# Optimization experiments

Hardware: AMD Instinct MI355X
Metric: run time of the kernel (lower is better)

## Reference

```python
import jax, jax.numpy as jnp
import numpy as np

N = 65536        # total nodes
E = 2097152      # total edges (avg degree 32)
B = 1024         # graphs / proteins
FXD = 78         # atom feature dim
DIM = 32         # GIN hidden dim
EMB = 128        # protein embedding dim
OUTD = 128       # output_dim
VOCAB = 26       # CHARPROTLEN + 1
PLEN = 1000      # protein sequence length (conv in_channels)
KS = 8           # conv kernel size
CLEN = EMB - KS + 1  # 121
NF = 32          # n_filters


def setup_inputs() -> dict:
    key = jax.random.key(0)
    ks = jax.random.split(key, 30)
    g = lambda k, s: (jax.random.normal(k, s, dtype=jnp.float32) * 0.05)
    inp = {
        "x": jax.random.normal(ks[0], (N, FXD), dtype=jnp.float32),
        "edge_index": jax.random.randint(ks[1], (2, E), 0, N, dtype=jnp.int32),
        "batch": jnp.sort(jax.random.randint(ks[2], (N,), 0, B, dtype=jnp.int32)),
        "target": jax.random.randint(ks[3], (B, PLEN), 0, VOCAB, dtype=jnp.int32),
        # GIN layer 1 MLP
        "w1a": g(ks[4], (FXD, DIM)), "b1a": jnp.zeros((DIM,), jnp.float32),
        "w1b": g(ks[5], (DIM, DIM)), "b1b": jnp.zeros((DIM,), jnp.float32),
        # GIN layers 2-5 MLPs (stacked)
        "wa": g(ks[6], (4, DIM, DIM)), "ba": jnp.zeros((4, DIM), jnp.float32),
        "wb": g(ks[7], (4, DIM, DIM)), "bb": jnp.zeros((4, DIM), jnp.float32),
        # BatchNorm affine params for bn1..bn5
        "gamma": jnp.ones((5, DIM), jnp.float32),
        "beta": jnp.zeros((5, DIM), jnp.float32),
        # drug head
        "w_fcxd": g(ks[8], (DIM, OUTD)), "b_fcxd": jnp.zeros((OUTD,), jnp.float32),
        # protein branch
        "emb": g(ks[9], (VOCAB, EMB)),
        "conv_w": g(ks[10], (NF, PLEN, KS)),  # OIH layout
        "conv_b": jnp.zeros((NF,), jnp.float32),
        "w_fcxt": g(ks[11], (NF * CLEN, OUTD)), "b_fcxt": jnp.zeros((OUTD,), jnp.float32),
        # joint head
        "w_fc1": g(ks[12], (256, 1024)), "b_fc1": jnp.zeros((1024,), jnp.float32),
        "w_fc2": g(ks[13], (1024, 256)), "b_fc2": jnp.zeros((256,), jnp.float32),
        "w_out": g(ks[14], (256, 1)), "b_out": jnp.zeros((1,), jnp.float32),
    }
    return inp


def reference(x, edge_index, batch, target,
              w1a, b1a, w1b, b1b, wa, ba, wb, bb, gamma, beta,
              w_fcxd, b_fcxd, emb, conv_w, conv_b, w_fcxt, b_fcxt,
              w_fc1, b_fc1, w_fc2, b_fc2, w_out, b_out):
    n_nodes = x.shape[0]
    n_graphs = target.shape[0]
    src, dst = edge_index[0], edge_index[1]

    def gin_bn(h, wi, bi, wo, bo, g, bt):
        # GINConv (eps=0): nn((1+eps)*x + sum_{j->i} x_j), then ReLU, then BatchNorm1d (batch stats)
        agg = jax.ops.segment_sum(h[src], dst, num_segments=n_nodes) + h
        h = jnp.maximum(agg @ wi + bi, 0.0) @ wo + bo
        h = jnp.maximum(h, 0.0)
        m = h.mean(axis=0)
        v = h.var(axis=0)  # biased, matches torch BN normalization
        return g * (h - m) * jax.lax.rsqrt(v + 1e-5) + bt

    h = gin_bn(x, w1a, b1a, w1b, b1b, gamma[0], beta[0])
    for i in range(4):
        h = gin_bn(h, wa[i], ba[i], wb[i], bb[i], gamma[i + 1], beta[i + 1])

    # global add pool over graphs
    hg = jax.ops.segment_sum(h, batch, num_segments=n_graphs)  # [B, 32]
    xd = jnp.maximum(hg @ w_fcxd + b_fcxd, 0.0)  # [B, 128] (dropout inactive in eval)

    # protein branch: embed then Conv1d over the embedding axis (in_channels = seq positions)
    e = emb[target]  # [B, 1000, 128]
    c = jax.lax.conv_general_dilated(e, conv_w, window_strides=(1,), padding="VALID",
                                     dimension_numbers=("NCH", "OIH", "NCH"))
    c = c + conv_b[None, :, None]  # [B, 32, 121]
    xt = c.reshape(n_graphs, NF * CLEN) @ w_fcxt + b_fcxt  # [B, 128], no activation in original

    xc = jnp.concatenate([xd, xt], axis=1)  # [B, 256]
    xc = jnp.maximum(xc @ w_fc1 + b_fc1, 0.0)
    xc = jnp.maximum(xc @ w_fc2 + b_fc2, 0.0)
    return xc @ w_out + b_out  # [B, 1]
```

## Files before the change

### kernel.cpp

```cpp
#include <hip/hip_runtime.h>
#include <hip/hip_fp16.h>

#define N_NODES 65536
#define N_EDGES 2097152
#define NB      1024
#define FXD     78
#define DIM     32
#define EMBD    128
#define OUTD    128
#define VOCAB   26
#define PLEN    1000
#define KS      8
#define CLEN    121
#define NF      32
#define FCX     (NF*CLEN)
#define NBKT    256
#define EPB     8192
#define NSLICE  256
#define EROW2   156
#define ECHUNK  13


__global__ __launch_bounds__(256) void k_bhist(
    const int* __restrict__ ei, int* __restrict__ bktCnt)
{
    __shared__ int h[NBKT];
    int tid = threadIdx.x;
    h[tid] = 0;
    __syncthreads();
    int base = blockIdx.x*1024;
    #pragma unroll
    for (int q=0; q<4; ++q) {
        int d = ei[N_EDGES + base + q*256 + tid];
        atomicAdd(&h[d>>8], 1);
    }
    __syncthreads();
    atomicAdd(&bktCnt[tid], h[tid]);
}

__global__ __launch_bounds__(256) void k_bscan(
    const int* __restrict__ bktCnt, int* __restrict__ bktBase, int* __restrict__ bktCur)
{
    __shared__ int s[NBKT];
    int t = threadIdx.x;
    int v = bktCnt[t];
    s[t] = v;
    __syncthreads();
    for (int off=1; off<256; off<<=1) {
        int tv = (t >= off) ? s[t-off] : 0;
        __syncthreads();
        s[t] += tv;
        __syncthreads();
    }
    int ex = s[t] - v;
    bktBase[t] = ex;
    bktCur[t] = ex;
    if (t == 255) bktBase[256] = s[255];
}

__global__ __launch_bounds__(256) void k_bucketA(
    const int* __restrict__ ei, int* __restrict__ bktCur, unsigned int* __restrict__ pairs)
{
    __shared__ unsigned int raw[EPB];
    __shared__ unsigned int srt[EPB];
    __shared__ unsigned char bOf[EPB];
    __shared__ int hist[NBKT], sc[NBKT], lcur[NBKT], gbase[NBKT];
    int tid = threadIdx.x;
    hist[tid] = 0;
    __syncthreads();
    int eb = blockIdx.x * EPB;
    for (int i=tid; i<EPB; i+=256) {
        int s = ei[eb+i];
        int d = ei[N_EDGES+eb+i];
        raw[i] = ((unsigned int)d<<16) | (unsigned int)s;
        atomicAdd(&hist[d>>8], 1);
    }
    __syncthreads();
    int v = hist[tid];
    sc[tid] = v;
    __syncthreads();
    for (int off=1; off<256; off<<=1) {
        int tv = (tid >= off) ? sc[tid-off] : 0;
        __syncthreads();
        sc[tid] += tv;
        __syncthreads();
    }
    int ex = sc[tid] - v;
    sc[tid] = ex;
    lcur[tid] = ex;
    gbase[tid] = atomicAdd(&bktCur[tid], v);
    __syncthreads();
    for (int i=tid; i<EPB; i+=256) {
        unsigned int p = raw[i];
        int k = p >> 24;
        int pos = atomicAdd(&lcur[k], 1);
        srt[pos] = p;
        bOf[pos] = (unsigned char)k;
    }
    __syncthreads();
    for (int i=tid; i<EPB; i+=256) {
        int k = bOf[i];
        pairs[gbase[k] + (i - sc[k])] = srt[i];
    }
}

__global__ __launch_bounds__(256) void k_fillB(
    const int* __restrict__ bktBase, const unsigned int* __restrict__ pairs,
    int* __restrict__ rowptr, int* __restrict__ csr)
{
    __shared__ int hist[256], sc[256], cur[256];
    int b = blockIdx.x, tid = threadIdx.x;
    int node0 = b*256;
    hist[tid] = 0;
    __syncthreads();
    int s = bktBase[b], e = bktBase[b+1];
    for (int i = s + tid; i < e; i += 256)
        atomicAdd(&hist[(pairs[i] >> 16) & 255], 1);
    __syncthreads();
    int v = hist[tid];
    sc[tid] = v;
    __syncthreads();
    for (int off=1; off<256; off<<=1) {
        int tv = (tid >= off) ? sc[tid-off] : 0;
        __syncthreads();
        sc[tid] += tv;
        __syncthreads();
    }
    int base = s + sc[tid] - v;
    rowptr[node0 + tid] = base;
    cur[tid] = base;
    if (b == NBKT-1 && tid == 255) rowptr[N_NODES] = N_EDGES;
    __syncthreads();
    for (int i = s + tid; i < e; i += 256) {
        unsigned int p = pairs[i];
        int pos = atomicAdd(&cur[(p >> 16) & 255], 1);
        csr[pos] = (int)(p & 0xFFFFu);
    }
}


__global__ __launch_bounds__(256) void k_l1_transform(
    const float* __restrict__ x, const float* __restrict__ w,
    __half* __restrict__ t)
{
    __shared__ float wS[FXD*DIM];
    for (int i = threadIdx.x; i < FXD*DIM; i += 256) wS[i] = w[i];
    __syncthreads();
    int node = blockIdx.x*256 + threadIdx.x;
    float acc[DIM];
    #pragma unroll
    for (int d=0; d<DIM; ++d) acc[d] = 0.f;
    const float* xr = x + (long)node*FXD;
    for (int j=0; j<FXD; ++j) {
        float xv = xr[j];
        #pragma unroll
        for (int d=0; d<DIM; ++d) acc[d] += xv * wS[j*DIM+d];
    }
    union { __half2 h2[16]; uint4 u4[4]; } pk;
    #pragma unroll
    for (int q=0; q<16; ++q) pk.h2[q] = __floats2half2_rn(acc[2*q], acc[2*q+1]);
    uint4* dst4 = (uint4*)(t + (long)node*DIM);
    #pragma unroll
    for (int q=0; q<4; ++q) dst4[q] = pk.u4[q];
}

__global__ __launch_bounds__(256) void k_transform(
    const float* __restrict__ z, const float* __restrict__ ss,
    const float* __restrict__ w, __half* __restrict__ t)
{
    __shared__ float wS[DIM*DIM];
    __shared__ float sS[2*DIM];
    for (int i = threadIdx.x; i < DIM*DIM; i += 256) wS[i] = w[i];
    if (threadIdx.x < 2*DIM) sS[threadIdx.x] = ss[threadIdx.x];
    __syncthreads();
    int node = blockIdx.x*256 + threadIdx.x;
    float h[DIM];
    const float4* z4 = (const float4*)(z + (long)node*DIM);
    #pragma unroll
    for (int q=0; q<DIM/4; ++q) {
        float4 v = z4[q];
        h[q*4+0]=v.x; h[q*4+1]=v.y; h[q*4+2]=v.z; h[q*4+3]=v.w;
    }
    #pragma unroll
    for (int d=0; d<DIM; ++d) h[d] = h[d]*sS[d] + sS[DIM+d];
    float acc[DIM];
    #pragma unroll
    for (int d=0; d<DIM; ++d) acc[d] = 0.f;
    #pragma unroll
    for (int j=0; j<DIM; ++j) {
        float hv = h[j];
        #pragma unroll
        for (int d=0; d<DIM; ++d) acc[d] += hv * wS[j*DIM+d];
    }
    union { __half2 h2[16]; uint4 u4[4]; } pk;
    #pragma unroll
    for (int q=0; q<16; ++q) pk.h2[q] = __floats2half2_rn(acc[2*q], acc[2*q+1]);
    uint4* dst4 = (uint4*)(t + (long)node*DIM);
    #pragma unroll
    for (int q=0; q<4; ++q) dst4[q] = pk.u4[q];
}

__global__ __launch_bounds__(256) void k_gather_mlp(
    const int* __restrict__ rowptr, const int* __restrict__ csr,
    const __half* __restrict__ t,
    const float* __restrict__ bi, const float* __restrict__ wo, const float* __restrict__ bo,
    float* __restrict__ z, float* __restrict__ part)
{
    __shared__ float wS[DIM*DIM];
    __shared__ float bS[2*DIM];
    __shared__ float stS[2*DIM];
    int tid = threadIdx.x;
    for (int i=tid; i<DIM*DIM; i+=256) wS[i]=wo[i];
    if (tid<DIM) bS[tid]=bi[tid];
    else if (tid<2*DIM) bS[tid]=bo[tid-DIM];
    if (tid<2*DIM) stS[tid]=0.f;
    __syncthreads();
    int g = tid >> 3;
    int l = tid & 7;
    int node = blockIdx.x*32 + g;
    const uint2* t4 = (const uint2*)t;
    uint2 sv = t4[(long)node*8 + l];
    float2 p0 = __half22float2(*(const __half2*)&sv.x);
    float2 p1 = __half22float2(*(const __half2*)&sv.y);
    float a0=p0.x, a1=p0.y, a2=p1.x, a3=p1.y;
    float c0=0.f, c1=0.f, c2=0.f, c3=0.f;
    int s0 = rowptr[node], s1 = rowptr[node+1];
    int e = s0;
    for (; e+8 <= s1; e+=8) {
        int myIdx = csr[e + l];
        #pragma unroll
        for (int k=0; k<8; ++k) {
            int idx = __shfl(myIdx, k, 8);
            uint2 v = t4[(long)idx*8 + l];
            float2 q0 = __half22float2(*(const __half2*)&v.x);
            float2 q1 = __half22float2(*(const __half2*)&v.y);
            if (k & 1) { c0+=q0.x; c1+=q0.y; c2+=q1.x; c3+=q1.y; }
            else       { a0+=q0.x; a1+=q0.y; a2+=q1.x; a3+=q1.y; }
        }
    }
    if (e+4 <= s1) {
        int myIdx = csr[e + (l & 3)];
        #pragma unroll
        for (int k=0; k<4; ++k) {
            int idx = __shfl(myIdx, k, 8);
            uint2 v = t4[(long)idx*8 + l];
            float2 q0 = __half22float2(*(const __half2*)&v.x);
            float2 q1 = __half22float2(*(const __half2*)&v.y);
            if (k & 1) { c0+=q0.x; c1+=q0.y; c2+=q1.x; c3+=q1.y; }
            else       { a0+=q0.x; a1+=q0.y; a2+=q1.x; a3+=q1.y; }
        }
        e += 4;
    }
    for (; e<s1; ++e) {
        uint2 v = t4[(long)csr[e]*8 + l];
        float2 q0 = __half22float2(*(const __half2*)&v.x);
        float2 q1 = __half22float2(*(const __half2*)&v.y);
        a0+=q0.x; a1+=q0.y; a2+=q1.x; a3+=q1.y;
    }
    float ua[4];
    ua[0] = fmaxf(a0+c0 + bS[4*l+0], 0.f);
    ua[1] = fmaxf(a1+c1 + bS[4*l+1], 0.f);
    ua[2] = fmaxf(a2+c2 + bS[4*l+2], 0.f);
    ua[3] = fmaxf(a3+c3 + bS[4*l+3], 0.f);
    float zz[4];
    #pragma unroll
    for (int q=0; q<4; ++q) zz[q] = bS[DIM + 4*l + q];
    const float4* w4 = (const float4*)wS;
    #pragma unroll
    for (int j=0; j<DIM; ++j) {
        float uj = __shfl(ua[j & 3], j >> 2, 8);
        float4 wv = w4[j*8 + l];
        zz[0]+=uj*wv.x; zz[1]+=uj*wv.y; zz[2]+=uj*wv.z; zz[3]+=uj*wv.w;
    }
    #pragma unroll
    for (int q=0; q<4; ++q) zz[q] = fmaxf(zz[q], 0.f);
    ((float4*)z)[(long)node*8 + l] = make_float4(zz[0], zz[1], zz[2], zz[3]);
    float sr[4], qr[4];
    #pragma unroll
    for (int q=0; q<4; ++q) { sr[q] = zz[q]; qr[q] = zz[q]*zz[q]; }
    #pragma unroll
    for (int q=0; q<4; ++q) {
        sr[q] += __shfl_down(sr[q], 32, 64); qr[q] += __shfl_down(qr[q], 32, 64);
        sr[q] += __shfl_down(sr[q], 16, 64); qr[q] += __shfl_down(qr[q], 16, 64);
        sr[q] += __shfl_down(sr[q],  8, 64); qr[q] += __shfl_down(qr[q],  8, 64);
    }
    if ((tid & 63) < 8) {
        #pragma unroll
        for (int q=0; q<4; ++q) {
            atomicAdd(&stS[4*l+q],       sr[q]);
            atomicAdd(&stS[DIM+4*l+q],   qr[q]);
        }
    }
    __syncthreads();
    if (tid < 2*DIM)
        atomicAdd(&part[((blockIdx.x & (NSLICE-1))<<6) + tid], stS[tid]);
}

__global__ __launch_bounds__(256) void k_scaleshift(
    float* __restrict__ part,
    const float* __restrict__ gamma, const float* __restrict__ beta,
    int layer, float* __restrict__ ss)
{
    __shared__ float red[4][64];
    __shared__ float totS[64];
    int t = threadIdx.x;
    int ch = t & 63, q = t >> 6;
    float s = 0.f;
    for (int i = q*64; i < q*64 + 64; ++i) s += part[(i<<6) + ch];
    red[q][ch] = s;
    __syncthreads();
    if (t < 64) totS[t] = red[0][t]+red[1][t]+red[2][t]+red[3][t];
    __syncthreads();
    if (t < DIM) {
        float mean = totS[t] * (1.f/N_NODES);
        float var  = totS[DIM+t] * (1.f/N_NODES) - mean*mean;
        float sc = gamma[layer*DIM+t] * rsqrtf(var + 1e-5f);
        ss[t] = sc;
        ss[DIM+t] = beta[layer*DIM+t] - mean*sc;
    }
    for (int i = t; i < NSLICE*64; i += 256) part[i] = 0.f;
}

__global__ __launch_bounds__(256) void k_pool(
    const float* __restrict__ z, const float* __restrict__ ss,
    const int* __restrict__ batch, float* __restrict__ hg)
{
    int tid = threadIdx.x;
    int node = blockIdx.x*32 + (tid>>3);
    int cq = tid & 7;
    float4 v = ((const float4*)z)[(long)node*8 + cq];
    float4 sc = ((const float4*)ss)[cq];
    float4 sh = ((const float4*)ss)[8 + cq];
    v.x = v.x*sc.x + sh.x; v.y = v.y*sc.y + sh.y;
    v.z = v.z*sc.z + sh.z; v.w = v.w*sc.w + sh.w;
    int b = batch[node];
    int b0 = __shfl(b, 0, 64);
    int b7 = __shfl(b, 63, 64);
    if (b0 == b7) {
        #pragma unroll
        for (int off=8; off<64; off<<=1) {
            v.x += __shfl_xor(v.x, off, 64);
            v.y += __shfl_xor(v.y, off, 64);
            v.z += __shfl_xor(v.z, off, 64);
            v.w += __shfl_xor(v.w, off, 64);
        }
        if ((tid & 63) < 8) {
            float* dst = hg + (long)b0*DIM + cq*4;
            atomicAdd(dst+0, v.x); atomicAdd(dst+1, v.y);
            atomicAdd(dst+2, v.z); atomicAdd(dst+3, v.w);
        }
    } else {
        float* dst = hg + (long)b*DIM + cq*4;
        atomicAdd(dst+0, v.x); atomicAdd(dst+1, v.y);
        atomicAdd(dst+2, v.z); atomicAdd(dst+3, v.w);
    }
}

__global__ __launch_bounds__(128) void k_xd(
    const float* __restrict__ hg, const float* __restrict__ w,
    const float* __restrict__ bias, float* __restrict__ xc)
{
    int b = blockIdx.x, n = threadIdx.x;
    __shared__ float hS[DIM];
    if (n < DIM) hS[n] = hg[b*DIM+n];
    __syncthreads();
    float acc = bias[n];
    #pragma unroll
    for (int r=0; r<DIM; ++r) acc += hS[r]*w[r*OUTD+n];
    xc[b*256 + n] = fmaxf(acc, 0.f);
}


__global__ __launch_bounds__(256) void k_cw_transpose(
    const float* __restrict__ cw, __half* __restrict__ cwT)
{
    int g = blockIdx.x*256 + threadIdx.x;
    int i = g >> 8;
    int j = g & 255;
    int o = j >> 3, k = j & 7;
    cwT[g] = __float2half(cw[o*(PLEN*KS) + i*KS + k]);
}

__global__ __launch_bounds__(256) void k_conv(
    const int* __restrict__ target, const float* __restrict__ emb,
    const __half* __restrict__ cwTh, const float* __restrict__ conv_b,
    float* __restrict__ c)
{
    __shared__ __align__(16) float Gs[VOCAB*256];
    __shared__ __align__(16) float U[2080];
    __shared__ int meta[3*VOCAB+2];
    __shared__ float cbS[NF];
    int* sortedS = (int*)U;
    int* cntS = meta;
    int* segS = meta + VOCAB;
    int* curS = meta + 2*VOCAB + 1;
    int b = blockIdx.x, j = threadIdx.x;
    if (j < VOCAB) cntS[j] = 0;
    if (j < NF) cbS[j] = conv_b[j];
    __syncthreads();
    int tloc[4];
    #pragma unroll
    for (int q=0; q<4; ++q) {
        int i = j + q*256;
        if (i < PLEN) {
            tloc[q] = target[b*PLEN+i];
            atomicAdd(&cntS[tloc[q]], 1);
        } else tloc[q] = -1;
    }
    __syncthreads();
    if (j == 0) {
        int run = 0;
        for (int v=0; v<VOCAB; ++v) { segS[v]=run; run += cntS[v]; }
        segS[VOCAB] = run;
    }
    __syncthreads();
    if (j < VOCAB) curS[j] = segS[j];
    __syncthreads();
    #pragma unroll
    for (int q=0; q<4; ++q) {
        int i = j + q*256;
        if (i < PLEN) {
            int pos = atomicAdd(&curS[tloc[q]], 1);
            sortedS[pos] = i;
        }
    }
    __syncthreads();
    int w = j >> 6;
    int lane = j & 63;
    int half32 = lane >> 5;
    int c32 = lane & 31;
    const uint4* cw4 = (const uint4*)cwTh;
    __half2 hz = __float2half2_rn(0.f);
    for (int v=0; v<VOCAB; ++v) {
        int s = segS[v], e2 = segS[v+1];
        int wv = s / 250; if (wv > 3) wv = 3;
        if (wv != w) continue;
        float facc[8];
        #pragma unroll
        for (int q=0; q<8; ++q) facc[q] = 0.f;
        int p = s;
        for (; p+16 <= e2; p += 16) {
            __half2 h0=hz, h1=hz, h2=hz, h3=hz;
            #pragma unroll
            for (int u=0; u<8; ++u) {
                int i0 = sortedS[p+2*u], i1 = sortedS[p+2*u+1];
                int row = half32 ? i1 : i0;
                uint4 q4 = cw4[row*32 + c32];
                const __half2* hh = (const __half2*)&q4;
                h0 = __hadd2(h0, hh[0]); h1 = __hadd2(h1, hh[1]);
                h2 = __hadd2(h2, hh[2]); h3 = __hadd2(h3, hh[3]);
            }
            float2 f0=__half22float2(h0), f1=__half22float2(h1),
                   f2=__half22float2(h2), f3=__half22float2(h3);
            facc[0]+=f0.x; facc[1]+=f0.y; facc[2]+=f1.x; facc[3]+=f1.y;
            facc[4]+=f2.x; facc[5]+=f2.y; facc[6]+=f3.x; facc[7]+=f3.y;
        }
        for (; p+2 <= e2; p += 2) {
            int i0 = sortedS[p], i1 = sortedS[p+1];
            int row = half32 ? i1 : i0;
            uint4 q4 = cw4[row*32 + c32];
            const __half2* hh = (const __half2*)&q4;
            float2 f0=__half22float2(hh[0]), f1=__half22float2(hh[1]),
                   f2=__half22float2(hh[2]), f3=__half22float2(hh[3]);
            facc[0]+=f0.x; facc[1]+=f0.y; facc[2]+=f1.x; facc[3]+=f1.y;
            facc[4]+=f2.x; facc[5]+=f2.y; facc[6]+=f3.x; facc[7]+=f3.y;
        }
        if (p < e2 && half32 == 0) {
            uint4 q4 = cw4[sortedS[p]*32 + c32];
            const __half2* hh = (const __half2*)&q4;
            float2 f0=__half22float2(hh[0]), f1=__half22float2(hh[1]),
                   f2=__half22float2(hh[2]), f3=__half22float2(hh[3]);
            facc[0]+=f0.x; facc[1]+=f0.y; facc[2]+=f1.x; facc[3]+=f1.y;
            facc[4]+=f2.x; facc[5]+=f2.y; facc[6]+=f3.x; facc[7]+=f3.y;
        }
        #pragma unroll
        for (int q=0; q<8; ++q) facc[q] += __shfl_xor(facc[q], 32, 64);
        if (half32 == 0) {
            float4* gp = (float4*)(Gs + v*256 + c32*8);
            gp[0] = make_float4(facc[0], facc[1], facc[2], facc[3]);
            gp[1] = make_float4(facc[4], facc[5], facc[6], facc[7]);
        }
    }
    int o = j >> 3, pg = j & 7;
    int t0 = pg*16;
    int tcnt = (t0+16 <= CLEN) ? 16 : (CLEN - t0);
    float out[16];
    #pragma unroll
    for (int q=0; q<16; ++q) out[q] = cbS[o];
    for (int ch=0; ch<2; ++ch) {
        __syncthreads();
        for (int i=j; i<ECHUNK*EMBD; i+=256) {
            int v = i >> 7, tt = i & 127;
            U[v*EROW2 + tt + 4*(tt>>4)] = emb[(ch*ECHUNK + v)*EMBD + tt];
        }
        __syncthreads();
        for (int vv=0; vv<ECHUNK; ++vv) {
            const float4* gp = (const float4*)(Gs + (ch*ECHUNK+vv)*256 + o*8);
            float4 g0 = gp[0], g1 = gp[1];
            float g[8] = {g0.x,g0.y,g0.z,g0.w,g1.x,g1.y,g1.z,g1.w};
            const float* ev = &U[vv*EROW2 + 20*pg];
            float4 E0 = *(const float4*)(ev);
            float4 E1 = *(const float4*)(ev+4);
            float4 E2 = *(const float4*)(ev+8);
            float4 E3 = *(const float4*)(ev+12);
            float4 E4 = *(const float4*)(ev+20);
            float4 E5 = *(const float4*)(ev+24);
            float e[24] = {E0.x,E0.y,E0.z,E0.w, E1.x,E1.y,E1.z,E1.w,
                           E2.x,E2.y,E2.z,E2.w, E3.x,E3.y,E3.z,E3.w,
                           E4.x,E4.y,E4.z,E4.w, E5.x,E5.y,E5.z,E5.w};
            #pragma unroll
            for (int q=0; q<16; ++q) {
                float s = 0.f;
                #pragma unroll
                for (int k=0; k<KS; ++k) s += e[q+k]*g[k];
                out[q] += s;
            }
        }
    }
    __syncthreads();
    float* stage = Gs;
    for (int q=0; q<tcnt; ++q) stage[o*CLEN + t0 + q] = out[q];
    __syncthreads();
    for (int idx=j; idx<FCX; idx+=256)
        c[(long)b*FCX + idx] = stage[idx];
}

#define XT_GB  16
#define XT_NS  16
#define XT_KS  (FCX/XT_NS)
#define XT_BK  22
#define XT_NCH (XT_KS/XT_BK)
__global__ __launch_bounds__(256) void k_xt(
    const float* __restrict__ c, const float* __restrict__ w,
    float* __restrict__ xtp)
{
    __shared__ float cS[XT_GB][XT_BK];
    __shared__ float wS[XT_BK][128];
    int b0 = blockIdx.x * XT_GB;
    int ks0 = blockIdx.y * XT_KS;
    int tid = threadIdx.x;
    int g2 = tid >> 5;
    int co = tid & 31;
    int cg0 = tid / XT_BK, ck0 = tid - cg0*XT_BK;
    int i1 = tid + 256;
    int cg1 = i1 / XT_BK, ck1 = i1 - cg1*XT_BK;
    float wreg[11], creg0, creg1;
    {
        int k0 = ks0;
        #pragma unroll
        for (int q=0; q<11; ++q) {
            int idx = tid + q*256;
            wreg[q] = w[(long)(k0 + (idx>>7))*OUTD + (idx & 127)];
        }
        creg0 = c[(long)(b0+cg0)*FCX + k0 + ck0];
        if (tid < 96) creg1 = c[(long)(b0+cg1)*FCX + k0 + ck1];
    }
    float acc[2][4];
    #pragma unroll
    for (int q=0; q<2; ++q)
      #pragma unroll
      for (int p=0; p<4; ++p) acc[q][p] = 0.f;
    for (int ch=0; ch<XT_NCH; ++ch) {
        #pragma unroll
        for (int q=0; q<11; ++q) {
            int idx = tid + q*256;
            wS[idx>>7][idx & 127] = wreg[q];
        }
        cS[cg0][ck0] = creg0;
        if (tid < 96) cS[cg1][ck1] = creg1;
        __syncthreads();
        if (ch+1 < XT_NCH) {
            int k0 = ks0 + (ch+1)*XT_BK;
            #pragma unroll
            for (int q=0; q<11; ++q) {
                int idx = tid + q*256;
                wreg[q] = w[(long)(k0 + (idx>>7))*OUTD + (idx & 127)];
            }
            creg0 = c[(long)(b0+cg0)*FCX + k0 + ck0];
            if (tid < 96) creg1 = c[(long)(b0+cg1)*FCX + k0 + ck1];
        }
        #pragma unroll
        for (int k2=0; k2<XT_BK/2; ++k2) {
            float2 cv0 = *(const float2*)&cS[2*g2  ][2*k2];
            float2 cv1 = *(const float2*)&cS[2*g2+1][2*k2];
            float4 wv0 = *(const float4*)&wS[2*k2  ][co*4];
            float4 wv1 = *(const float4*)&wS[2*k2+1][co*4];
            acc[0][0]+=cv0.x*wv0.x; acc[0][1]+=cv0.x*wv0.y;
            acc[0][2]+=cv0.x*wv0.z; acc[0][3]+=cv0.x*wv0.w;
            acc[1][0]+=cv1.x*wv0.x; acc[1][1]+=cv1.x*wv0.y;
            acc[1][2]+=cv1.x*wv0.z; acc[1][3]+=cv1.x*wv0.w;
            acc[0][0]+=cv0.y*wv1.x; acc[0][1]+=cv0.y*wv1.y;
            acc[0][2]+=cv0.y*wv1.z; acc[0][3]+=cv0.y*wv1.w;
            acc[1][0]+=cv1.y*wv1.x; acc[1][1]+=cv1.y*wv1.y;
            acc[1][2]+=cv1.y*wv1.z; acc[1][3]+=cv1.y*wv1.w;
        }
        __syncthreads();
    }
    #pragma unroll
    for (int q=0; q<2; ++q) {
        int g = b0 + 2*g2 + q;
        float4* dst = (float4*)(xtp + ((long)blockIdx.y*NB + g)*128);
        dst[co] = make_float4(acc[q][0], acc[q][1], acc[q][2], acc[q][3]);
    }
}

__global__ __launch_bounds__(256) void k_xt_red(
    const float* __restrict__ xtp, const float* __restrict__ bias,
    float* __restrict__ xc)
{
    int p = blockIdx.x*256 + threadIdx.x;
    int g = p >> 5, c4 = p & 31;
    const float4* src = (const float4*)xtp;
    float4 s = src[(long)g*32 + c4];
    #pragma unroll
    for (int y=1; y<XT_NS; ++y) {
        float4 v = src[((long)y*NB + g)*32 + c4];
        s.x += v.x; s.y += v.y; s.z += v.z; s.w += v.w;
    }
    float4 bv = ((const float4*)bias)[c4];
    s.x += bv.x; s.y += bv.y; s.z += bv.z; s.w += bv.w;
    ((float4*)(xc + g*256 + 128))[c4] = s;
}


#define FC1_NS 4
#define FC1_KR 64
__global__ __launch_bounds__(256) void k_fc1(
    const float* __restrict__ xc, const float* __restrict__ w,
    float* __restrict__ y1p)
{
    __shared__ float xS[4][FC1_KR];
    int b0 = blockIdx.x*4;
    int r0 = blockIdx.y*FC1_KR;
    int n = threadIdx.x;
    xS[n>>6][n&63] = xc[(b0 + (n>>6))*256 + r0 + (n&63)];
    __syncthreads();
    float acc[4][4];
    #pragma unroll
    for (int q=0;q<4;++q)
      #pragma unroll
      for (int m=0;m<4;++m) acc[q][m]=0.f;
    for (int r=0; r<FC1_KR; ++r) {
        float x0=xS[0][r], x1=xS[1][r], x2=xS[2][r], x3=xS[3][r];
        #pragma unroll
        for (int m=0; m<4; ++m) {
            float wv = w[(long)(r0+r)*1024 + m*256 + n];
            acc[0][m]+=x0*wv; acc[1][m]+=x1*wv;
            acc[2][m]+=x2*wv; acc[3][m]+=x3*wv;
        }
    }
    long base = ((long)blockIdx.y*NB + b0)*1024;
    #pragma unroll
    for (int q=0; q<4; ++q)
        #pragma unroll
        for (int m=0; m<4; ++m)
            y1p[base + (long)q*1024 + m*256 + n] = acc[q][m];
}

__global__ __launch_bounds__(256) void k_fc1_red(
    const float* __restrict__ y1p, const float* __restrict__ bias,
    float* __restrict__ y)
{
    int p = blockIdx.x*256 + threadIdx.x;
    int g = p >> 8, c4 = p & 255;
    const float4* src = (const float4*)y1p;
    float4 s = src[(long)g*256 + c4];
    #pragma unroll
    for (int yq=1; yq<FC1_NS; ++yq) {
        float4 v = src[((long)yq*NB + g)*256 + c4];
        s.x+=v.x; s.y+=v.y; s.z+=v.z; s.w+=v.w;
    }
    float4 bv = ((const float4*)bias)[c4];
    s.x = fmaxf(s.x+bv.x, 0.f); s.y = fmaxf(s.y+bv.y, 0.f);
    s.z = fmaxf(s.z+bv.z, 0.f); s.w = fmaxf(s.w+bv.w, 0.f);
    ((float4*)y)[(long)g*256 + c4] = s;
}

#define FC2_NS 8
#define FC2_KR 128
__global__ __launch_bounds__(256) void k_fc2(
    const float* __restrict__ y, const float* __restrict__ w,
    float* __restrict__ y2p)
{
    __shared__ float xS[4][FC2_KR];
    int b0 = blockIdx.x*4;
    int r0 = blockIdx.y*FC2_KR;
    int n = threadIdx.x;
    {
        int e1 = n + 256;
        xS[n>>7][n&127]   = y[(b0 + (n>>7))*1024  + r0 + (n&127)];
        xS[e1>>7][e1&127] = y[(b0 + (e1>>7))*1024 + r0 + (e1&127)];
    }
    __syncthreads();
    float acc[4] = {0.f, 0.f, 0.f, 0.f};
    for (int r=0; r<FC2_KR; ++r) {
        float wv = w[(long)(r0+r)*256 + n];
        acc[0]+=xS[0][r]*wv; acc[1]+=xS[1][r]*wv;
        acc[2]+=xS[2][r]*wv; acc[3]+=xS[3][r]*wv;
    }
    long base = ((long)blockIdx.y*NB + b0)*256;
    #pragma unroll
    for (int q=0; q<4; ++q) y2p[base + q*256 + n] = acc[q];
}

__global__ __launch_bounds__(256) void k_fc2_red(
    const float* __restrict__ y2p, const float* __restrict__ bias,
    float* __restrict__ y2)
{
    int p = blockIdx.x*256 + threadIdx.x;
    int g = p >> 6, c4 = p & 63;
    const float4* src = (const float4*)y2p;
    float4 s = src[(long)g*64 + c4];
    #pragma unroll
    for (int yq=1; yq<FC2_NS; ++yq) {
        float4 v = src[((long)yq*NB + g)*64 + c4];
        s.x+=v.x; s.y+=v.y; s.z+=v.z; s.w+=v.w;
    }
    float4 bv = ((const float4*)bias)[c4];
    s.x = fmaxf(s.x+bv.x, 0.f); s.y = fmaxf(s.y+bv.y, 0.f);
    s.z = fmaxf(s.z+bv.z, 0.f); s.w = fmaxf(s.w+bv.w, 0.f);
    ((float4*)y2)[(long)g*64 + c4] = s;
}

__global__ __launch_bounds__(256) void k_out(
    const float* __restrict__ y2, const float* __restrict__ w,
    const float* __restrict__ bias, float* __restrict__ out)
{
    int b = blockIdx.x, n = threadIdx.x;
    float v = y2[b*256 + n] * w[n];
    #pragma unroll
    for (int off=32; off; off>>=1) v += __shfl_down(v, off, 64);
    __shared__ float red[4];
    if ((n & 63) == 0) red[n >> 6] = v;
    __syncthreads();
    if (n == 0) out[b] = red[0]+red[1]+red[2]+red[3] + bias[0];
}


extern "C" void kernel_launch(void* const* d_in, const int* in_sizes, int n_in,
                              void* d_out, int out_size, void* d_ws, size_t ws_size,
                              hipStream_t stream) {
    const float* x      = (const float*)d_in[0];
    const int*   ei     = (const int*)  d_in[1];
    const int*   batch  = (const int*)  d_in[2];
    const int*   target = (const int*)  d_in[3];
    const float* w1a    = (const float*)d_in[4];
    const float* b1a    = (const float*)d_in[5];
    const float* w1b    = (const float*)d_in[6];
    const float* b1b    = (const float*)d_in[7];
    const float* wa     = (const float*)d_in[8];
    const float* ba     = (const float*)d_in[9];
    const float* wb     = (const float*)d_in[10];
    const float* bb     = (const float*)d_in[11];
    const float* gamma  = (const float*)d_in[12];
    const float* beta   = (const float*)d_in[13];
    const float* w_fcxd = (const float*)d_in[14];
    const float* b_fcxd = (const float*)d_in[15];
    const float* emb    = (const float*)d_in[16];
    const float* conv_w = (const float*)d_in[17];
    const float* conv_b = (const float*)d_in[18];
    const float* w_fcxt = (const float*)d_in[19];
    const float* b_fcxt = (const float*)d_in[20];
    const float* w_fc1  = (const float*)d_in[21];
    const float* b_fc1  = (const float*)d_in[22];
    const float* w_fc2  = (const float*)d_in[23];
    const float* b_fc2  = (const float*)d_in[24];
    const float* w_out  = (const float*)d_in[25];
    const float* b_out  = (const float*)d_in[26];

    float* ws      = (float*)d_ws;
    __half* tH     = (__half*)ws;
    float* z       = ws + 1048576;
    unsigned int* pairs = (unsigned int*)(z + (size_t)N_NODES*DIM);
    int*   csr     = (int*)(pairs + N_EDGES);
    int*   rowptr  = csr + N_EDGES;
    int*   bktCnt  = rowptr + (N_NODES + 8);
    int*   bktBase = bktCnt + 256;
    int*   bktCur  = bktBase + 264;
    float* ss      = (float*)(bktCur + 256);
    float* hg      = ss + 64;
    float* cwT     = hg + (size_t)NB*DIM;
    float* cbuf    = cwT + 256000;
    float* xc      = cbuf + (size_t)NB*FCX;
    float* y1      = xc + (size_t)NB*256;
    float* y2      = y1 + (size_t)NB*1024;
    float* part    = y2 + (size_t)NB*256;
    __half* cwTh   = (__half*)cwT;
    float* xtp     = z;
    float* y1p     = ws;
    float* y2p     = ws + 4194304;

    hipMemsetAsync(bktCnt, 0, 256*sizeof(int), stream);
    k_bhist<<<N_EDGES/1024, 256, 0, stream>>>(ei, bktCnt);
    k_bscan<<<1, 256, 0, stream>>>(bktCnt, bktBase, bktCur);
    k_bucketA<<<NBKT, 256, 0, stream>>>(ei, bktCur, pairs);
    k_fillB<<<NBKT, 256, 0, stream>>>(bktBase, pairs, rowptr, csr);

    k_cw_transpose<<<1000, 256, 0, stream>>>(conv_w, cwTh);
    k_conv<<<NB, 256, 0, stream>>>(target, emb, cwTh, conv_b, cbuf);
    k_xt<<<dim3(NB/XT_GB, XT_NS), 256, 0, stream>>>(cbuf, w_fcxt, xtp);
    k_xt_red<<<(NB*DIM)/256, 256, 0, stream>>>(xtp, b_fcxt, xc);

    hipMemsetAsync(part, 0, NSLICE*64*sizeof(float), stream);
    for (int l=0; l<5; ++l) {
        if (l == 0)
            k_l1_transform<<<N_NODES/256, 256, 0, stream>>>(x, w1a, tH);
        else
            k_transform<<<N_NODES/256, 256, 0, stream>>>(z, ss, wa + (size_t)(l-1)*DIM*DIM, tH);
        const float* bi = (l==0) ? b1a : ba + (size_t)(l-1)*DIM;
        const float* wo = (l==0) ? w1b : wb + (size_t)(l-1)*DIM*DIM;
        const float* bo = (l==0) ? b1b : bb + (size_t)(l-1)*DIM;
        k_gather_mlp<<<N_NODES/32, 256, 0, stream>>>(rowptr, csr, tH, bi, wo, bo, z, part);
        k_scaleshift<<<1, 256, 0, stream>>>(part, gamma, beta, l, ss);
    }

    hipMemsetAsync(hg, 0, (size_t)NB*DIM*sizeof(float), stream);
    k_pool<<<N_NODES/32, 256, 0, stream>>>(z, ss, batch, hg);
    k_xd<<<NB, 128, 0, stream>>>(hg, w_fcxd, b_fcxd, xc);

    k_fc1<<<dim3(NB/4, FC1_NS), 256, 0, stream>>>(xc, w_fc1, y1p);
    k_fc1_red<<<1024, 256, 0, stream>>>(y1p, b_fc1, y1);
    k_fc2<<<dim3(NB/4, FC2_NS), 256, 0, stream>>>(y1, w_fc2, y2p);
    k_fc2_red<<<256, 256, 0, stream>>>(y2p, b_fc2, y2);
    k_out<<<NB, 256, 0, stream>>>(y2, w_out, b_out, (float*)d_out);
}
```

Measured before the change: 686.5 us.

## Split conv into vocab-table and convolution kernels; fold BN stats into transform

```diff
diff --git a/kernel.cpp b/kernel.cpp
--- a/kernel.cpp
+++ b/kernel.cpp
@@ -165,15 +165,33 @@
 }
 
 __global__ __launch_bounds__(256) void k_transform(
-    const float* __restrict__ z, const float* __restrict__ ss,
+    const float* __restrict__ z, const float* __restrict__ part,
+    const float* __restrict__ gamma, const float* __restrict__ beta, int layer,
     const float* __restrict__ w, __half* __restrict__ t)
 {
     __shared__ float wS[DIM*DIM];
+    __shared__ float red[4][64];
     __shared__ float sS[2*DIM];
-    for (int i = threadIdx.x; i < DIM*DIM; i += 256) wS[i] = w[i];
-    if (threadIdx.x < 2*DIM) sS[threadIdx.x] = ss[threadIdx.x];
-    __syncthreads();
-    int node = blockIdx.x*256 + threadIdx.x;
+    int tid = threadIdx.x;
+    for (int i=tid; i<DIM*DIM; i+=256) wS[i] = w[i];
+    {
+        int ch = tid & 63, qq = tid >> 6;
+        float s = 0.f;
+        for (int i = qq*64; i < qq*64 + 64; ++i) s += part[(i<<6) + ch];
+        red[qq][ch] = s;
+    }
+    __syncthreads();
+    if (tid < DIM) {
+        float tots = red[0][tid]+red[1][tid]+red[2][tid]+red[3][tid];
+        float totq = red[0][DIM+tid]+red[1][DIM+tid]+red[2][DIM+tid]+red[3][DIM+tid];
+        float mean = tots * (1.f/N_NODES);
+        float var  = totq * (1.f/N_NODES) - mean*mean;
+        float sc = gamma[layer*DIM+tid] * rsqrtf(var + 1e-5f);
+        sS[tid] = sc;
+        sS[DIM+tid] = beta[layer*DIM+tid] - mean*sc;
+    }
+    __syncthreads();
+    int node = blockIdx.x*256 + tid;
     float h[DIM];
     const float4* z4 = (const float4*)(z + (long)node*DIM);
     #pragma unroll
@@ -297,7 +315,7 @@
 }
 
 __global__ __launch_bounds__(256) void k_scaleshift(
-    float* __restrict__ part,
+    const float* __restrict__ part,
     const float* __restrict__ gamma, const float* __restrict__ beta,
     int layer, float* __restrict__ ss)
 {
@@ -318,7 +336,6 @@
         ss[t] = sc;
         ss[DIM+t] = beta[layer*DIM+t] - mean*sc;
     }
-    for (int i = t; i < NSLICE*64; i += 256) part[i] = 0.f;
 }
 
 __global__ __launch_bounds__(256) void k_pool(
@@ -381,22 +398,18 @@
     cwT[g] = __float2half(cw[o*(PLEN*KS) + i*KS + k]);
 }
 
-__global__ __launch_bounds__(256) void k_conv(
-    const int* __restrict__ target, const float* __restrict__ emb,
-    const __half* __restrict__ cwTh, const float* __restrict__ conv_b,
-    float* __restrict__ c)
-{
-    __shared__ __align__(16) float Gs[VOCAB*256];
-    __shared__ __align__(16) float U[2080];
+__global__ __launch_bounds__(256) void k_convA(
+    const int* __restrict__ target, const __half* __restrict__ cwTh,
+    __half* __restrict__ G)
+{
+    __shared__ int sortedS[PLEN];
     __shared__ int meta[3*VOCAB+2];
-    __shared__ float cbS[NF];
-    int* sortedS = (int*)U;
     int* cntS = meta;
     int* segS = meta + VOCAB;
     int* curS = meta + 2*VOCAB + 1;
-    int b = blockIdx.x, j = threadIdx.x;
+    int bb = blockIdx.x, j = threadIdx.x;
+    int b = bb >> 1, sub = bb & 1;
     if (j < VOCAB) cntS[j] = 0;
-    if (j < NF) cbS[j] = conv_b[j];
     __syncthreads();
     int tloc[4];
     #pragma unroll
@@ -431,9 +444,13 @@
     int c32 = lane & 31;
     const uint4* cw4 = (const uint4*)cwTh;
     __half2 hz = __float2half2_rn(0.f);
-    for (int v=0; v<VOCAB; ++v) {
+    int v0 = 13*sub, v1 = v0 + 13;
+    int segbase = segS[v0];
+    int tot = segS[v1] - segbase;
+    for (int v=v0; v<v1; ++v) {
         int s = segS[v], e2 = segS[v+1];
-        int wv = s / 250; if (wv > 3) wv = 3;
+        int wv = (tot > 0) ? ((s - segbase)*4)/tot : 0;
+        if (wv > 3) wv = 3;
         if (wv != w) continue;
         float facc[8];
         #pragma unroll
@@ -476,15 +493,39 @@
         #pragma unroll
         for (int q=0; q<8; ++q) facc[q] += __shfl_xor(facc[q], 32, 64);
         if (half32 == 0) {
-            float4* gp = (float4*)(Gs + v*256 + c32*8);
-            gp[0] = make_float4(facc[0], facc[1], facc[2], facc[3]);
-            gp[1] = make_float4(facc[4], facc[5], facc[6], facc[7]);
-        }
+            __half2 o0 = __floats2half2_rn(facc[0], facc[1]);
+            __half2 o1 = __floats2half2_rn(facc[2], facc[3]);
+            __half2 o2 = __floats2half2_rn(facc[4], facc[5]);
+            __half2 o3 = __floats2half2_rn(facc[6], facc[7]);
+            uint4 pk;
+            pk.x = *(unsigned int*)&o0; pk.y = *(unsigned int*)&o1;
+            pk.z = *(unsigned int*)&o2; pk.w = *(unsigned int*)&o3;
+            ((uint4*)(G + ((long)b*VOCAB + v)*256))[c32] = pk;
+        }
+    }
+}
+
+__global__ __launch_bounds__(256) void k_convB(
+    const float* __restrict__ emb, const __half* __restrict__ G,
+    const float* __restrict__ conv_b, float* __restrict__ c)
+{
+    __shared__ __align__(16) char buf[21632];
+    __shared__ float cbS[NF];
+    __half* GsH = (__half*)buf;
+    float*  U   = (float*)(buf + 13312);
+    float*  stage = (float*)buf;
+    int b = blockIdx.x, j = threadIdx.x;
+    if (j < NF) cbS[j] = conv_b[j];
+    {
+        const uint4* gsrc = (const uint4*)(G + (long)b*VOCAB*256);
+        uint4* gdst = (uint4*)GsH;
+        for (int i=j; i<832; i+=256) gdst[i] = gsrc[i];
     }
     int o = j >> 3, pg = j & 7;
     int t0 = pg*16;
     int tcnt = (t0+16 <= CLEN) ? 16 : (CLEN - t0);
     float out[16];
+    __syncthreads();
     #pragma unroll
     for (int q=0; q<16; ++q) out[q] = cbS[o];
     for (int ch=0; ch<2; ++ch) {
@@ -495,9 +536,11 @@
         }
         __syncthreads();
         for (int vv=0; vv<ECHUNK; ++vv) {
-            const float4* gp = (const float4*)(Gs + (ch*ECHUNK+vv)*256 + o*8);
-            float4 g0 = gp[0], g1 = gp[1];
-            float g[8] = {g0.x,g0.y,g0.z,g0.w,g1.x,g1.y,g1.z,g1.w};
+            uint4 gv = *(const uint4*)(GsH + (ch*ECHUNK+vv)*256 + o*8);
+            const __half2* gh = (const __half2*)&gv;
+            float2 ga = __half22float2(gh[0]), gb = __half22float2(gh[1]);
+            float2 gc = __half22float2(gh[2]), gd = __half22float2(gh[3]);
+            float g[8] = {ga.x,ga.y,gb.x,gb.y,gc.x,gc.y,gd.x,gd.y};
             const float* ev = &U[vv*EROW2 + 20*pg];
             float4 E0 = *(const float4*)(ev);
             float4 E1 = *(const float4*)(ev+4);
@@ -518,7 +561,6 @@
         }
     }
     __syncthreads();
-    float* stage = Gs;
     for (int q=0; q<tcnt; ++q) stage[o*CLEN + t0 + q] = out[q];
     __syncthreads();
     for (int idx=j; idx<FCX; idx+=256)
@@ -787,6 +829,7 @@
     float* part    = y2 + (size_t)NB*256;
     __half* cwTh   = (__half*)cwT;
     float* xtp     = z;
+    __half* Gbuf   = (__half*)z;
     float* y1p     = ws;
     float* y2p     = ws + 4194304;
 
@@ -797,22 +840,26 @@
     k_fillB<<<NBKT, 256, 0, stream>>>(bktBase, pairs, rowptr, csr);
 
     k_cw_transpose<<<1000, 256, 0, stream>>>(conv_w, cwTh);
-    k_conv<<<NB, 256, 0, stream>>>(target, emb, cwTh, conv_b, cbuf);
+    k_convA<<<2*NB, 256, 0, stream>>>(target, cwTh, Gbuf);
+    k_convB<<<NB, 256, 0, stream>>>(emb, Gbuf, conv_b, cbuf);
     k_xt<<<dim3(NB/XT_GB, XT_NS), 256, 0, stream>>>(cbuf, w_fcxt, xtp);
     k_xt_red<<<(NB*DIM)/256, 256, 0, stream>>>(xtp, b_fcxt, xc);
 
-    hipMemsetAsync(part, 0, NSLICE*64*sizeof(float), stream);
+    hipMemsetAsync(part, 0, 5*NSLICE*64*sizeof(float), stream);
     for (int l=0; l<5; ++l) {
         if (l == 0)
             k_l1_transform<<<N_NODES/256, 256, 0, stream>>>(x, w1a, tH);
         else
-            k_transform<<<N_NODES/256, 256, 0, stream>>>(z, ss, wa + (size_t)(l-1)*DIM*DIM, tH);
+            k_transform<<<N_NODES/256, 256, 0, stream>>>(
+                z, part + (size_t)(l-1)*NSLICE*64, gamma, beta, l-1,
+                wa + (size_t)(l-1)*DIM*DIM, tH);
         const float* bi = (l==0) ? b1a : ba + (size_t)(l-1)*DIM;
         const float* wo = (l==0) ? w1b : wb + (size_t)(l-1)*DIM*DIM;
         const float* bo = (l==0) ? b1b : bb + (size_t)(l-1)*DIM;
-        k_gather_mlp<<<N_NODES/32, 256, 0, stream>>>(rowptr, csr, tH, bi, wo, bo, z, part);
-        k_scaleshift<<<1, 256, 0, stream>>>(part, gamma, beta, l, ss);
-    }
+        k_gather_mlp<<<N_NODES/32, 256, 0, stream>>>(
+            rowptr, csr, tH, bi, wo, bo, z, part + (size_t)l*NSLICE*64);
+    }
+    k_scaleshift<<<1, 256, 0, stream>>>(part + (size_t)4*NSLICE*64, gamma, beta, 4, ss);
 
     hipMemsetAsync(hg, 0, (size_t)NB*DIM*sizeof(float), stream);
     k_pool<<<N_NODES/32, 256, 0, stream>>>(z, ss, batch, hg);
```

Measured after the change: 670.3 us. 1.02x faster.
